# Optimization experiments

Measured on AMD Instinct MI355X. Metric: run time of the kernel, lower is better.

The kernel has to match this reference:

```python
import jax, jax.numpy as jnp
import numpy as np

B, T, N = 64, 128, 64   # batch, win_size, input_size (= node_num)
H, E, K, CS = 64, 128, 7, 8  # hidden_size, embed_size, kernel_size, control_size
NEG_SLOPE = 0.2


def _p(key, shape, scale=0.05):
    return scale * jax.random.normal(key, shape, dtype=jnp.float32)


def setup_inputs() -> dict:
    key = jax.random.key(0)
    ks = jax.random.split(key, 32)
    inp = {
        "x": jax.random.normal(ks[0], (B, T, N), dtype=jnp.float32),
        "y": jax.random.normal(ks[1], (B, T, CS), dtype=jnp.float32),
        # Conv1d(N -> N, kernel K)
        "conv_w": _p(ks[2], (N, N, K)),
        "conv_b": _p(ks[3], (N,)),
        # rnn_enc GRU: input N -> hidden H
        "We_ih": _p(ks[4], (3 * H, N)), "We_hh": _p(ks[5], (3 * H, H)),
        "be_ih": _p(ks[6], (3 * H,)), "be_hh": _p(ks[7], (3 * H,)),
        # MP_GAT linears
        "Ww": _p(ks[8], (E, 2 * T)), "bw": _p(ks[9], (E,)),
        "Wa": _p(ks[10], (1, E)), "ba": _p(ks[11], (1,)),
        # encoder GRU: input H+N -> H
        "Wm_ih": _p(ks[12], (3 * H, H + N)), "Wm_hh": _p(ks[13], (3 * H, H)),
        "bm_ih": _p(ks[14], (3 * H,)), "bm_hh": _p(ks[15], (3 * H,)),
        # rnn_dec GRU: input H -> H
        "Wd_ih": _p(ks[16], (3 * H, H)), "Wd_hh": _p(ks[17], (3 * H, H)),
        "bd_ih": _p(ks[18], (3 * H,)), "bd_hh": _p(ks[19], (3 * H,)),
        # fc_dec: H -> N
        "W_dec": _p(ks[20], (N, H)), "b_dec": _p(ks[21], (N,)),
        # fc_pred: Linear(H,N), ReLU, Linear(N,N)
        "W_p1": _p(ks[22], (N, H)), "b_p1": _p(ks[23], (N,)),
        "W_p2": _p(ks[24], (N, N)), "b_p2": _p(ks[25], (N,)),
    }
    return inp


def gru_seq(x_seq, Wih, Whh, bih, bhh):
    """torch nn.GRU (batch_first, h0=0). x_seq: [B,T,in] -> [B,T,H]."""
    gi = jnp.einsum('bti,gi->btg', x_seq, Wih) + bih  # [B,T,3H] (precompute input proj)
    h0 = jnp.zeros((x_seq.shape[0], Whh.shape[1]), x_seq.dtype)

    def step(h, gi_t):
        gh = h @ Whh.T + bhh
        i_r, i_z, i_n = jnp.split(gi_t, 3, axis=-1)
        h_r, h_z, h_n = jnp.split(gh, 3, axis=-1)
        r = jax.nn.sigmoid(i_r + h_r)
        z = jax.nn.sigmoid(i_z + h_z)
        n = jnp.tanh(i_n + r * h_n)
        h_new = (1.0 - z) * n + z * h
        return h_new, h_new

    _, hs = jax.lax.scan(step, h0, jnp.swapaxes(gi, 0, 1))
    return jnp.swapaxes(hs, 0, 1)


def _forward(x, y, conv_w, conv_b, We_ih, We_hh, be_ih, be_hh, Ww, bw, Wa, ba,
             Wm_ih, Wm_hh, bm_ih, bm_hh, Wd_ih, Wd_hh, bd_ih, bd_hh,
             W_dec, b_dec, W_p1, b_p1, W_p2, b_p2):
    # ---- CNN: pad 'same' + Conv1d + SELU. x: [B,T,N] -> channels first [B,N,T]
    pad = (K - 1) // 2
    xc = jnp.swapaxes(x, 1, 2)
    c = jax.lax.conv_general_dilated(xc, conv_w, (1,), [(pad, pad)],
                                     dimension_numbers=('NCH', 'OIH', 'NCH'))
    c = jax.nn.selu(c + conv_b[None, :, None])  # [B,N,T]
    c_btn = jnp.swapaxes(c, 1, 2)               # [B,T,N]

    # ---- rnn_enc GRU over time
    h_out = gru_seq(c_btn, We_ih, We_hh, be_ih, be_hh)  # [B,T,H]

    # ---- MP_GAT on c (v: [B, node, seq] = [B,N,T])
    v = c
    vi = jnp.broadcast_to(v[:, :, None, :], (B, N, N, T))
    vj = jnp.broadcast_to(v[:, None, :, :], (B, N, N, T))
    v_cat = jnp.concatenate([vi, vj], axis=-1)          # [B,N,N,2T]
    x_w = jax.nn.leaky_relu(jnp.einsum('bijt,et->bije', v_cat, Ww) + bw, NEG_SLOPE)
    e = (jnp.einsum('bije,oe->bijo', x_w, Wa) + ba)[..., 0]  # [B,N,N]
    attention = jax.nn.softmax(e, axis=2)
    # dropout is identity in eval mode
    h_mp = jax.nn.sigmoid(jnp.einsum('bij,bjt->bit', attention, v))  # [B,N,T]
    h_mp = jnp.swapaxes(h_mp, 1, 2)                      # [B,T,N]

    # ---- encoder / decoder GRUs (dropout = identity in eval)
    h_cat = jnp.concatenate([h_out, h_mp], axis=2)       # [B,T,H+N]
    h_enc = gru_seq(h_cat, Wm_ih, Wm_hh, bm_ih, bm_hh)
    h_dec = gru_seq(h_enc, Wd_ih, Wd_hh, bd_ih, bd_hh)

    recon = h_dec @ W_dec.T + b_dec                      # [B,T,N]
    p = jax.nn.relu(h_dec[:, 0, :] @ W_p1.T + b_p1)
    pred = p @ W_p2.T + b_p2                             # [B,N]
    return recon, pred


def reference(x, y, conv_w, conv_b, We_ih, We_hh, be_ih, be_hh, Ww, bw, Wa, ba,
              Wm_ih, Wm_hh, bm_ih, bm_hh, Wd_ih, Wd_hh, bd_ih, bd_hh,
              W_dec, b_dec, W_p1, b_p1, W_p2, b_p2):
    return _forward(x, y, conv_w, conv_b, We_ih, We_hh, be_ih, be_hh, Ww, bw, Wa, ba,
                    Wm_ih, Wm_hh, bm_ih, bm_hh, Wd_ih, Wd_hh, bd_ih, bd_hh,
                    W_dec, b_dec, W_p1, b_p1, W_p2, b_p2)
```

## Files before the change

kernel.cpp:

```cpp
#include <hip/hip_runtime.h>
#include <math.h>

#define BB 64
#define TT 128
#define NN 64
#define HH 64
#define EE 128
#define KK 7
#define GG 192

typedef _Float16 half2_t __attribute__((ext_vector_type(2)));

__device__ __forceinline__ float sigmoidf_(float x){ return 1.f/(1.f+expf(-x)); }
__device__ __forceinline__ float fsig_(float x){
  return __builtin_amdgcn_rcpf(1.f + __builtin_amdgcn_exp2f(-1.44269504f * x));
}
__device__ __forceinline__ float ftanh_(float x){
  return fmaf(-2.f, __builtin_amdgcn_rcpf(1.f + __builtin_amdgcn_exp2f(2.88539008f * x)), 1.f);
}

#define PIPE_BARRIER() asm volatile("s_waitcnt lgkmcnt(0)\ns_barrier" ::: "memory")
#define LGKM0() asm volatile("s_waitcnt lgkmcnt(0)" ::: "memory")

__device__ __forceinline__ void loadrow_(float* d, const float* src){
  const float4* p = (const float4*)src;
  #pragma unroll
  for (int i = 0; i < 16; ++i) {
    float4 v = p[i];
    d[4*i] = v.x; d[4*i+1] = v.y; d[4*i+2] = v.z; d[4*i+3] = v.w;
  }
}
__device__ __forceinline__ void loadroww_(half2_t* d, const float* src){
  const float4* p = (const float4*)src;
  #pragma unroll
  for (int i = 0; i < 16; ++i) {
    float4 v = p[i];
    d[2*i]   = half2_t{(_Float16)v.x, (_Float16)v.y};
    d[2*i+1] = half2_t{(_Float16)v.z, (_Float16)v.w};
  }
}

__global__ void conv_selu_kernel(const float* __restrict__ x, const float* __restrict__ w,
                                 const float* __restrict__ bias,
                                 float* __restrict__ c_nt, float* __restrict__ c_btn) {
  const int og = blockIdx.x, b = blockIdx.y, t = threadIdx.x;
  const int o0 = og * 8;
  __shared__ __align__(16) float xs[NN][TT + 1];
  __shared__ __align__(16) float ws[NN * KK][8];
  for (int idx = t; idx < TT * NN; idx += 128) {
    int tt = idx >> 6, nn = idx & 63;
    xs[nn][tt] = x[(size_t)(b * TT + tt) * NN + nn];
  }
  for (int idx = t; idx < NN * KK * 8; idx += 128) {
    int oo = idx & 7, ik = idx >> 3;
    ws[ik][oo] = w[(size_t)(o0 + oo) * (NN * KK) + ik];
  }
  __syncthreads();
  float acc[8];
  #pragma unroll
  for (int oo = 0; oo < 8; ++oo) acc[oo] = bias[o0 + oo];
  for (int i = 0; i < NN; ++i) {
    #pragma unroll
    for (int k = 0; k < KK; ++k) {
      int tt = t + k - 3;
      if (tt >= 0 && tt < TT) {
        float xv = xs[i][tt];
        const float* wp = &ws[i * KK + k][0];
        float4 w0 = *(const float4*)wp;
        float4 w1 = *(const float4*)(wp + 4);
        acc[0] += xv * w0.x; acc[1] += xv * w0.y; acc[2] += xv * w0.z; acc[3] += xv * w0.w;
        acc[4] += xv * w1.x; acc[5] += xv * w1.y; acc[6] += xv * w1.z; acc[7] += xv * w1.w;
      }
    }
  }
  const float alpha = 1.6732632423543772f, scale = 1.0507009873554805f;
  #pragma unroll
  for (int oo = 0; oo < 8; ++oo) {
    float a = acc[oo];
    float r = a > 0.f ? scale * a : scale * alpha * expm1f(a);
    int o = o0 + oo;
    c_nt[((size_t)b * NN + o) * TT + t] = r;
    c_btn[((size_t)b * TT + t) * NN + o] = r;
  }
}

__global__ void s12_kernel(const float* __restrict__ c_nt, const float* __restrict__ Ww,
                           float* __restrict__ s1, float* __restrict__ s2) {
  const int m0 = blockIdx.x * 16, col = threadIdx.x;
  __shared__ __align__(16) float ins[16][TT];
  for (int idx = col; idx < 16 * TT; idx += 128) {
    int r = idx >> 7, k = idx & 127;
    ins[r][k] = c_nt[(size_t)(m0 + r) * TT + k];
  }
  __syncthreads();
  const float* w1 = Ww + (size_t)col * (2 * TT);
  const float* w2 = w1 + TT;
  float acc1[16], acc2[16];
  #pragma unroll
  for (int r = 0; r < 16; ++r) { acc1[r] = 0.f; acc2[r] = 0.f; }
  #pragma unroll 2
  for (int k = 0; k < TT; k += 4) {
    float4 wv1 = *(const float4*)(w1 + k);
    float4 wv2 = *(const float4*)(w2 + k);
    #pragma unroll
    for (int r = 0; r < 16; ++r) {
      float4 iv = *(const float4*)&ins[r][k];
      acc1[r] += iv.x * wv1.x + iv.y * wv1.y + iv.z * wv1.z + iv.w * wv1.w;
      acc2[r] += iv.x * wv2.x + iv.y * wv2.y + iv.z * wv2.z + iv.w * wv2.w;
    }
  }
  #pragma unroll
  for (int r = 0; r < 16; ++r) {
    s1[(size_t)(m0 + r) * EE + col] = acc1[r];
    s2[(size_t)(m0 + r) * EE + col] = acc2[r];
  }
}

__global__ void gat_kernel(const float* __restrict__ s1, const float* __restrict__ s2,
                           const float* __restrict__ bw, const float* __restrict__ Wa,
                           const float* __restrict__ ba, const float* __restrict__ c_nt,
                           float* __restrict__ hmp) {
  const int it = blockIdx.x, b = blockIdx.y, tid = threadIdx.x;
  const int i0 = it * 16;
  __shared__ float s2s[NN][EE + 1];
  __shared__ float s1b[16][EE];
  __shared__ float cs[NN][TT + 1];
  __shared__ float was[EE];
  __shared__ float att[16][NN];
  for (int idx = tid; idx < NN * EE; idx += 256) {
    int j = idx >> 7, e = idx & 127;
    s2s[j][e] = s2[((size_t)b * NN + j) * EE + e] + bw[e];
  }
  for (int idx = tid; idx < 16 * EE; idx += 256) {
    int r = idx >> 7, e = idx & 127;
    s1b[r][e] = s1[((size_t)b * NN + i0 + r) * EE + e];
  }
  for (int idx = tid; idx < NN * TT; idx += 256) {
    int j = idx >> 7, t = idx & 127;
    cs[j][t] = c_nt[((size_t)b * NN + j) * TT + t];
  }
  if (tid < EE) was[tid] = Wa[tid];
  __syncthreads();
  const int wv = tid >> 6, j = tid & 63;
  #pragma unroll
  for (int pass = 0; pass < 4; ++pass) {
    const int il = pass * 4 + wv;
    float acc = 0.f;
    #pragma unroll 8
    for (int e = 0; e < EE; ++e) {
      float v = s1b[il][e] + s2s[j][e];
      v = v > 0.f ? v : 0.2f * v;
      acc += was[e] * v;
    }
    float ej = acc + ba[0];
    float mx = ej;
    for (int off = 32; off >= 1; off >>= 1) mx = fmaxf(mx, __shfl_xor(mx, off));
    float ex = __builtin_amdgcn_exp2f(1.44269504f * (ej - mx));
    float sm = ex;
    for (int off = 32; off >= 1; off >>= 1) sm += __shfl_xor(sm, off);
    att[il][j] = ex / sm;
  }
  __syncthreads();
  for (int o = tid; o < 16 * TT; o += 256) {
    int il = o >> 7, t = o & 127;
    float acc = 0.f;
    #pragma unroll 8
    for (int jj = 0; jj < NN; ++jj) acc += att[il][jj] * cs[jj][t];
    hmp[((size_t)b * TT + t) * NN + i0 + il] = sigmoidf_(acc);
  }
}

__global__ __launch_bounds__(256, 1)
void fused_chain4(const float* __restrict__ c_btn, const float* __restrict__ hmp,
                  const float* __restrict__ We_ih, const float* __restrict__ be_ih,
                  const float* __restrict__ We_hh, const float* __restrict__ be_hh,
                  const float* __restrict__ Wm_ih, const float* __restrict__ bm_ih,
                  const float* __restrict__ Wm_hh, const float* __restrict__ bm_hh,
                  const float* __restrict__ Wd_ih, const float* __restrict__ bd_ih,
                  const float* __restrict__ Wd_hh, const float* __restrict__ bd_hh,
                  const float* __restrict__ W_dec, const float* __restrict__ b_dec,
                  const float* __restrict__ W_p1, const float* __restrict__ b_p1,
                  const float* __restrict__ W_p2, const float* __restrict__ b_p2,
                  float* __restrict__ recon, float* __restrict__ pred) {
  const int b = blockIdx.x, tid = threadIdx.x, wid = tid >> 6, g = tid & 63;
  __shared__ __align__(16) _Float16 cbuf[HH], mbuf[HH], h3h[HH];
  __shared__ __align__(16) _Float16 h1h[2][HH], h2h[2][HH];
  __shared__ __align__(16) float q2[2][GG], h3f[2][HH];
  __shared__ __align__(16) float h0s[HH], ps[HH];

  half2_t wxa[32], wxb[32], wxc[32];
  half2_t wya[32], wyb[32], wyc[32];
  float wdec[64];
  float b0 = 0.f, b1 = 0.f, b2 = 0.f, e0 = 0.f, e1 = 0.f, e2 = 0.f, bdc = 0.f;
  if (wid == 0) {
    loadroww_(wxa, We_ih + (size_t)g * HH);
    loadroww_(wxb, We_ih + (size_t)(g + 64) * HH);
    loadroww_(wxc, We_ih + (size_t)(g + 128) * HH);
    loadroww_(wya, We_hh + (size_t)g * HH);
    loadroww_(wyb, We_hh + (size_t)(g + 64) * HH);
    loadroww_(wyc, We_hh + (size_t)(g + 128) * HH);
    b0 = be_ih[g]; b1 = be_ih[64 + g]; b2 = be_ih[128 + g];
    e0 = be_hh[g]; e1 = be_hh[64 + g]; e2 = be_hh[128 + g];
  } else if (wid == 1) {
    loadroww_(wxa, Wm_ih + (size_t)g * 128);
    loadroww_(wxb, Wm_ih + (size_t)(g + 64) * 128);
    loadroww_(wxc, Wm_ih + (size_t)(g + 128) * 128);
    loadroww_(wya, Wm_ih + (size_t)g * 128 + 64);
    loadroww_(wyb, Wm_ih + (size_t)(g + 64) * 128 + 64);
    loadroww_(wyc, Wm_ih + (size_t)(g + 128) * 128 + 64);
    b0 = bm_ih[g]; b1 = bm_ih[64 + g]; b2 = bm_ih[128 + g];
  } else if (wid == 2) {
    loadroww_(wxa, Wm_hh + (size_t)g * HH);
    loadroww_(wxb, Wm_hh + (size_t)(g + 64) * HH);
    loadroww_(wxc, Wm_hh + (size_t)(g + 128) * HH);
    loadrow_(wdec, W_dec + (size_t)g * HH);
    b0 = bm_hh[g]; b1 = bm_hh[64 + g]; b2 = bm_hh[128 + g];
    bdc = b_dec[g];
  } else {
    loadroww_(wxa, Wd_ih + (size_t)g * HH);
    loadroww_(wxb, Wd_ih + (size_t)(g + 64) * HH);
    loadroww_(wxc, Wd_ih + (size_t)(g + 128) * HH);
    loadroww_(wya, Wd_hh + (size_t)g * HH);
    loadroww_(wyb, Wd_hh + (size_t)(g + 64) * HH);
    loadroww_(wyc, Wd_hh + (size_t)(g + 128) * HH);
    b0 = bd_ih[g]; b1 = bd_ih[64 + g]; b2 = bd_ih[128 + g];
    e0 = bd_hh[g]; e1 = bd_hh[64 + g]; e2 = bd_hh[128 + g];
  }
  if (wid == 0) {
    h1h[0][g] = (_Float16)0.f; h1h[1][g] = (_Float16)0.f;
    h2h[0][g] = (_Float16)0.f; h2h[1][g] = (_Float16)0.f;
    h3h[g]    = (_Float16)0.f;
  }
  const float* cb = c_btn + (size_t)b * TT * NN + g;
  const float* hm = hmp   + (size_t)b * TT * NN + g;
  float cc = 0.f, cn = 0.f;
  if (wid == 0) { cc = cb[0]; cn = cb[NN]; }
  if (wid == 1) { cc = hm[0]; cn = hm[NN]; }
  float hown = 0.f;
  __syncthreads();

  for (int p = 0; p < TT + 4; ++p) {
    const int pw = p & 1, pr = pw ^ 1;
    if (wid == 0) {
      int t = p;
      if (t < TT) {
        cbuf[g] = (_Float16)cc;
        float cl = 0.f;
        if (t + 2 < TT) cl = cb[(size_t)(t + 2) * NN];
        LGKM0();
        float a0 = b0, a1 = b1, a2 = b2, r0 = e0, r1 = e1, r2 = e2;
        const float4* c4 = (const float4*)&cbuf[0];
        const float4* h4 = (const float4*)&h1h[pr][0];
        #pragma unroll
        for (int ch = 0; ch < 8; ++ch) {
          float4 cv = c4[ch], hv = h4[ch];
          const half2_t* cq = (const half2_t*)&cv;
          const half2_t* hq = (const half2_t*)&hv;
          #pragma unroll
          for (int k = 0; k < 4; ++k) {
            int i = 4 * ch + k;
            a0 = __builtin_amdgcn_fdot2(cq[k], wxa[i], a0, false);
            a1 = __builtin_amdgcn_fdot2(cq[k], wxb[i], a1, false);
            a2 = __builtin_amdgcn_fdot2(cq[k], wxc[i], a2, false);
            r0 = __builtin_amdgcn_fdot2(hq[k], wya[i], r0, false);
            r1 = __builtin_amdgcn_fdot2(hq[k], wyb[i], r1, false);
            r2 = __builtin_amdgcn_fdot2(hq[k], wyc[i], r2, false);
          }
        }
        float r = fsig_(a0 + r0), z = fsig_(a1 + r1), n = ftanh_(a2 + r * r2);
        hown = fmaf(z, hown - n, n);
        h1h[pw][g] = (_Float16)hown;
        cc = cn; cn = cl;
      }
    } else if (wid == 1) {
      int t = p - 1;
      if (t >= 0 && t < TT) {
        mbuf[g] = (_Float16)cc;
        float cl = 0.f;
        if (t + 2 < TT) cl = hm[(size_t)(t + 2) * NN];
        LGKM0();
        float a0 = b0, a1 = b1, a2 = b2, r0 = 0.f, r1 = 0.f, r2 = 0.f;
        const float4* h4 = (const float4*)&h1h[pr][0];
        const float4* m4 = (const float4*)&mbuf[0];
        #pragma unroll
        for (int ch = 0; ch < 8; ++ch) {
          float4 hv = h4[ch], mv = m4[ch];
          const half2_t* hq = (const half2_t*)&hv;
          const half2_t* mq = (const half2_t*)&mv;
          #pragma unroll
          for (int k = 0; k < 4; ++k) {
            int i = 4 * ch + k;
            a0 = __builtin_amdgcn_fdot2(hq[k], wxa[i], a0, false);
            a1 = __builtin_amdgcn_fdot2(hq[k], wxb[i], a1, false);
            a2 = __builtin_amdgcn_fdot2(hq[k], wxc[i], a2, false);
            r0 = __builtin_amdgcn_fdot2(mq[k], wya[i], r0, false);
            r1 = __builtin_amdgcn_fdot2(mq[k], wyb[i], r1, false);
            r2 = __builtin_amdgcn_fdot2(mq[k], wyc[i], r2, false);
          }
        }
        q2[pw][g] = a0 + r0; q2[pw][64 + g] = a1 + r1; q2[pw][128 + g] = a2 + r2;
        cc = cn; cn = cl;
      }
    } else if (wid == 2) {
      int t = p - 2;
      if (t >= 0 && t < TT) {
        float a0 = b0, a1 = b1, a2 = b2;
        const float4* h4 = (const float4*)&h2h[pr][0];
        #pragma unroll
        for (int ch = 0; ch < 8; ++ch) {
          float4 hv = h4[ch];
          const half2_t* hq = (const half2_t*)&hv;
          #pragma unroll
          for (int k = 0; k < 4; ++k) {
            int i = 4 * ch + k;
            a0 = __builtin_amdgcn_fdot2(hq[k], wxa[i], a0, false);
            a1 = __builtin_amdgcn_fdot2(hq[k], wxb[i], a1, false);
            a2 = __builtin_amdgcn_fdot2(hq[k], wxc[i], a2, false);
          }
        }
        float r = fsig_(q2[pr][g] + a0), z = fsig_(q2[pr][64 + g] + a1);
        float n = ftanh_(q2[pr][128 + g] + r * a2);
        hown = fmaf(z, hown - n, n);
        h2h[pw][g] = (_Float16)hown;
      }
      int t4 = p - 4;
      if (t4 >= 0) {
        const float4* h4 = (const float4*)&h3f[pr][0];
        float a0 = bdc, a1 = 0.f;
        #pragma unroll
        for (int i = 0; i < 8; ++i) {
          float4 hv = h4[2 * i], hw = h4[2 * i + 1];
          a0 = fmaf(hv.x, wdec[8*i],   fmaf(hv.y, wdec[8*i+1], fmaf(hv.z, wdec[8*i+2], fmaf(hv.w, wdec[8*i+3], a0))));
          a1 = fmaf(hw.x, wdec[8*i+4], fmaf(hw.y, wdec[8*i+5], fmaf(hw.z, wdec[8*i+6], fmaf(hw.w, wdec[8*i+7], a1))));
        }
        recon[((size_t)b * TT + t4) * NN + g] = a0 + a1;
      }
    } else {
      int t = p - 3;
      if (t >= 0 && t < TT) {
        float a0 = b0, a1 = b1, a2 = b2, r0 = e0, r1 = e1, r2 = e2;
        const float4* h4 = (const float4*)&h2h[pr][0];
        const float4* o4 = (const float4*)&h3h[0];
        #pragma unroll
        for (int ch = 0; ch < 8; ++ch) {
          float4 hv = h4[ch], ov = o4[ch];
          const half2_t* hq = (const half2_t*)&hv;
          const half2_t* oq = (const half2_t*)&ov;
          #pragma unroll
          for (int k = 0; k < 4; ++k) {
            int i = 4 * ch + k;
            a0 = __builtin_amdgcn_fdot2(hq[k], wxa[i], a0, false);
            a1 = __builtin_amdgcn_fdot2(hq[k], wxb[i], a1, false);
            a2 = __builtin_amdgcn_fdot2(hq[k], wxc[i], a2, false);
            r0 = __builtin_amdgcn_fdot2(oq[k], wya[i], r0, false);
            r1 = __builtin_amdgcn_fdot2(oq[k], wyb[i], r1, false);
            r2 = __builtin_amdgcn_fdot2(oq[k], wyc[i], r2, false);
          }
        }
        float r = fsig_(a0 + r0), z = fsig_(a1 + r1), n = ftanh_(a2 + r * r2);
        hown = fmaf(z, hown - n, n);
        h3h[g] = (_Float16)hown;
        h3f[pw][g] = hown;
        if (t == 0) h0s[g] = hown;
      }
    }
    PIPE_BARRIER();
  }

  if (wid == 2) {
    float w1r[64]; loadrow_(w1r, W_p1 + (size_t)g * HH);
    const float4* h4 = (const float4*)&h0s[0];
    float a = b_p1[g];
    #pragma unroll
    for (int i = 0; i < 16; ++i) {
      float4 hv = h4[i];
      a = fmaf(hv.x, w1r[4*i], fmaf(hv.y, w1r[4*i+1], fmaf(hv.z, w1r[4*i+2], fmaf(hv.w, w1r[4*i+3], a))));
    }
    ps[g] = fmaxf(a, 0.f);
    LGKM0();
    float w2r[64]; loadrow_(w2r, W_p2 + (size_t)g * HH);
    const float4* p4 = (const float4*)&ps[0];
    float c2 = b_p2[g];
    #pragma unroll
    for (int i = 0; i < 16; ++i) {
      float4 pv = p4[i];
      c2 = fmaf(pv.x, w2r[4*i], fmaf(pv.y, w2r[4*i+1], fmaf(pv.z, w2r[4*i+2], fmaf(pv.w, w2r[4*i+3], c2))));
    }
    pred[(size_t)b * NN + g] = c2;
  }
}

extern "C" void kernel_launch(void* const* d_in, const int* in_sizes, int n_in,
                              void* d_out, int out_size, void* d_ws, size_t ws_size,
                              hipStream_t stream) {
  const float* x      = (const float*)d_in[0];
  const float* conv_w = (const float*)d_in[2];
  const float* conv_b = (const float*)d_in[3];
  const float* We_ih  = (const float*)d_in[4];
  const float* We_hh  = (const float*)d_in[5];
  const float* be_ih  = (const float*)d_in[6];
  const float* be_hh  = (const float*)d_in[7];
  const float* Ww     = (const float*)d_in[8];
  const float* bw     = (const float*)d_in[9];
  const float* Wa     = (const float*)d_in[10];
  const float* ba     = (const float*)d_in[11];
  const float* Wm_ih  = (const float*)d_in[12];
  const float* Wm_hh  = (const float*)d_in[13];
  const float* bm_ih  = (const float*)d_in[14];
  const float* bm_hh  = (const float*)d_in[15];
  const float* Wd_ih  = (const float*)d_in[16];
  const float* Wd_hh  = (const float*)d_in[17];
  const float* bd_ih  = (const float*)d_in[18];
  const float* bd_hh  = (const float*)d_in[19];
  const float* W_dec  = (const float*)d_in[20];
  const float* b_dec  = (const float*)d_in[21];
  const float* W_p1   = (const float*)d_in[22];
  const float* b_p1   = (const float*)d_in[23];
  const float* W_p2   = (const float*)d_in[24];
  const float* b_p2   = (const float*)d_in[25];
  float* out = (float*)d_out;

  float* wsf   = (float*)d_ws;
  float* c_nt  = wsf;
  float* c_btn = c_nt  + 524288;
  float* s1    = c_btn + 524288;
  float* s2    = s1    + 524288;
  float* hmp   = s2    + 524288;

  conv_selu_kernel<<<dim3(8, BB), 128, 0, stream>>>(x, conv_w, conv_b, c_nt, c_btn);
  s12_kernel<<<BB * NN / 16, 128, 0, stream>>>(c_nt, Ww, s1, s2);
  gat_kernel<<<dim3(4, BB), 256, 0, stream>>>(s1, s2, bw, Wa, ba, c_nt, hmp);
  fused_chain4<<<BB, 256, 0, stream>>>(c_btn, hmp,
                                       We_ih, be_ih, We_hh, be_hh,
                                       Wm_ih, bm_ih, Wm_hh, bm_hh,
                                       Wd_ih, bd_ih, Wd_hh, bd_hh,
                                       W_dec, b_dec, W_p1, b_p1, W_p2, b_p2,
                                       out, out + BB * TT * NN);
}
```

Measured before the change: 212.0 us.

## Process four timesteps per barrier phase in the fused GRU wavefront pipeline

The four-wave pipelined GRU chain now advances in chunks of four timesteps per block-wide barrier instead of one. This cuts the number of s_barrier phases from about TT+4 to about TT/4+4. Within a chunk, the serial waves read their own previous step from LDS with only an lgkmcnt wait, not a full barrier. Shared buffers grow to hold four steps per phase. The cost is a longer pipeline fill/drain and more LDS traffic per phase.

```diff
diff --git a/kernel.cpp b/kernel.cpp
--- a/kernel.cpp
+++ b/kernel.cpp
@@ -37,6 +37,46 @@
     float4 v = p[i];
     d[2*i]   = half2_t{(_Float16)v.x, (_Float16)v.y};
     d[2*i+1] = half2_t{(_Float16)v.z, (_Float16)v.w};
+  }
+}
+__device__ __forceinline__ void mv6_(const _Float16* xs, const _Float16* ys,
+    const half2_t* wxa, const half2_t* wxb, const half2_t* wxc,
+    const half2_t* wya, const half2_t* wyb, const half2_t* wyc,
+    float& a0, float& a1, float& a2, float& r0, float& r1, float& r2){
+  const float4* x4 = (const float4*)xs;
+  const float4* y4 = (const float4*)ys;
+  #pragma unroll
+  for (int ch = 0; ch < 8; ++ch) {
+    float4 xv = x4[ch], yv = y4[ch];
+    const half2_t* xq = (const half2_t*)&xv;
+    const half2_t* yq = (const half2_t*)&yv;
+    #pragma unroll
+    for (int k = 0; k < 4; ++k) {
+      int i = 4 * ch + k;
+      a0 = __builtin_amdgcn_fdot2(xq[k], wxa[i], a0, false);
+      a1 = __builtin_amdgcn_fdot2(xq[k], wxb[i], a1, false);
+      a2 = __builtin_amdgcn_fdot2(xq[k], wxc[i], a2, false);
+      r0 = __builtin_amdgcn_fdot2(yq[k], wya[i], r0, false);
+      r1 = __builtin_amdgcn_fdot2(yq[k], wyb[i], r1, false);
+      r2 = __builtin_amdgcn_fdot2(yq[k], wyc[i], r2, false);
+    }
+  }
+}
+__device__ __forceinline__ void mv3_(const _Float16* xs,
+    const half2_t* wxa, const half2_t* wxb, const half2_t* wxc,
+    float& a0, float& a1, float& a2){
+  const float4* x4 = (const float4*)xs;
+  #pragma unroll
+  for (int ch = 0; ch < 8; ++ch) {
+    float4 xv = x4[ch];
+    const half2_t* xq = (const half2_t*)&xv;
+    #pragma unroll
+    for (int k = 0; k < 4; ++k) {
+      int i = 4 * ch + k;
+      a0 = __builtin_amdgcn_fdot2(xq[k], wxa[i], a0, false);
+      a1 = __builtin_amdgcn_fdot2(xq[k], wxb[i], a1, false);
+      a2 = __builtin_amdgcn_fdot2(xq[k], wxc[i], a2, false);
+    }
   }
 }
 
@@ -170,23 +210,40 @@
   }
 }
 
+#define K4 4
 __global__ __launch_bounds__(256, 1)
-void fused_chain4(const float* __restrict__ c_btn, const float* __restrict__ hmp,
-                  const float* __restrict__ We_ih, const float* __restrict__ be_ih,
-                  const float* __restrict__ We_hh, const float* __restrict__ be_hh,
-                  const float* __restrict__ Wm_ih, const float* __restrict__ bm_ih,
-                  const float* __restrict__ Wm_hh, const float* __restrict__ bm_hh,
-                  const float* __restrict__ Wd_ih, const float* __restrict__ bd_ih,
-                  const float* __restrict__ Wd_hh, const float* __restrict__ bd_hh,
-                  const float* __restrict__ W_dec, const float* __restrict__ b_dec,
-                  const float* __restrict__ W_p1, const float* __restrict__ b_p1,
-                  const float* __restrict__ W_p2, const float* __restrict__ b_p2,
-                  float* __restrict__ recon, float* __restrict__ pred) {
+void fused_chain4k(const float* __restrict__ c_btn, const float* __restrict__ hmp,
+                   const float* __restrict__ We_ih, const float* __restrict__ be_ih,
+                   const float* __restrict__ We_hh, const float* __restrict__ be_hh,
+                   const float* __restrict__ Wm_ih, const float* __restrict__ bm_ih,
+                   const float* __restrict__ Wm_hh, const float* __restrict__ bm_hh,
+                   const float* __restrict__ Wd_ih, const float* __restrict__ bd_ih,
+                   const float* __restrict__ Wd_hh, const float* __restrict__ bd_hh,
+                   const float* __restrict__ W_dec, const float* __restrict__ b_dec,
+                   const float* __restrict__ W_p1, const float* __restrict__ b_p1,
+                   const float* __restrict__ W_p2, const float* __restrict__ b_p2,
+                   float* __restrict__ recon, float* __restrict__ pred) {
   const int b = blockIdx.x, tid = threadIdx.x, wid = tid >> 6, g = tid & 63;
-  __shared__ __align__(16) _Float16 cbuf[HH], mbuf[HH], h3h[HH];
-  __shared__ __align__(16) _Float16 h1h[2][HH], h2h[2][HH];
-  __shared__ __align__(16) float q2[2][GG], h3f[2][HH];
+  __shared__ __align__(16) _Float16 cbuf[2][K4][HH], mbuf[2][K4][HH];
+  __shared__ __align__(16) _Float16 h1h[2][K4][HH], h2h[2][K4][HH], h3h[2][K4][HH];
+  __shared__ __align__(16) float q2[2][K4][GG], h3f[2][K4][HH];
   __shared__ __align__(16) float h0s[HH], ps[HH];
+
+  {
+    _Float16* z1 = &h1h[0][0][0];
+    _Float16* z2 = &h2h[0][0][0];
+    _Float16* z3 = &h3h[0][0][0];
+    _Float16* z4 = &cbuf[0][0][0];
+    _Float16* z5 = &mbuf[0][0][0];
+    for (int idx = tid; idx < 2 * K4 * HH; idx += 256) {
+      z1[idx] = (_Float16)0.f; z2[idx] = (_Float16)0.f; z3[idx] = (_Float16)0.f;
+      z4[idx] = (_Float16)0.f; z5[idx] = (_Float16)0.f;
+    }
+    float* zf = &h3f[0][0][0];
+    for (int idx = tid; idx < 2 * K4 * HH; idx += 256) zf[idx] = 0.f;
+    float* zq = &q2[0][0][0];
+    for (int idx = tid; idx < 2 * K4 * GG; idx += 256) zq[idx] = 0.f;
+  }
 
   half2_t wxa[32], wxb[32], wxc[32];
   half2_t wya[32], wyb[32], wyc[32];
@@ -226,142 +283,109 @@
     b0 = bd_ih[g]; b1 = bd_ih[64 + g]; b2 = bd_ih[128 + g];
     e0 = bd_hh[g]; e1 = bd_hh[64 + g]; e2 = bd_hh[128 + g];
   }
-  if (wid == 0) {
-    h1h[0][g] = (_Float16)0.f; h1h[1][g] = (_Float16)0.f;
-    h2h[0][g] = (_Float16)0.f; h2h[1][g] = (_Float16)0.f;
-    h3h[g]    = (_Float16)0.f;
-  }
   const float* cb = c_btn + (size_t)b * TT * NN + g;
   const float* hm = hmp   + (size_t)b * TT * NN + g;
-  float cc = 0.f, cn = 0.f;
-  if (wid == 0) { cc = cb[0]; cn = cb[NN]; }
-  if (wid == 1) { cc = hm[0]; cn = hm[NN]; }
+  float cur[K4], nxt[K4];
+  #pragma unroll
+  for (int s = 0; s < K4; ++s) { cur[s] = 0.f; nxt[s] = 0.f; }
+  if (wid == 0) {
+    #pragma unroll
+    for (int s = 0; s < K4; ++s) cur[s] = cb[(size_t)s * NN];
+  }
+  if (wid == 1) {
+    #pragma unroll
+    for (int s = 0; s < K4; ++s) cur[s] = hm[(size_t)s * NN];
+  }
   float hown = 0.f;
   __syncthreads();
 
-  for (int p = 0; p < TT + 4; ++p) {
+  const int NPH = TT / K4 + 4;
+  for (int p = 0; p < NPH; ++p) {
     const int pw = p & 1, pr = pw ^ 1;
     if (wid == 0) {
-      int t = p;
-      if (t < TT) {
-        cbuf[g] = (_Float16)cc;
-        float cl = 0.f;
-        if (t + 2 < TT) cl = cb[(size_t)(t + 2) * NN];
+      if (p <= TT / K4 - 1) {
+        const int t0 = p * K4;
+        #pragma unroll
+        for (int s = 0; s < K4; ++s) cbuf[pw][s][g] = (_Float16)cur[s];
+        #pragma unroll
+        for (int s = 0; s < K4; ++s)
+          nxt[s] = (t0 + K4 + s < TT) ? cb[(size_t)(t0 + K4 + s) * NN] : 0.f;
+        #pragma unroll
+        for (int s = 0; s < K4; ++s) {
+          const _Float16* hp = (s == 0) ? &h1h[pr][K4-1][0] : &h1h[pw][s-1][0];
+          LGKM0();
+          float a0 = b0, a1 = b1, a2 = b2, r0 = e0, r1 = e1, r2 = e2;
+          mv6_(&cbuf[pw][s][0], hp, wxa, wxb, wxc, wya, wyb, wyc, a0, a1, a2, r0, r1, r2);
+          float r = fsig_(a0 + r0), z = fsig_(a1 + r1), n = ftanh_(a2 + r * r2);
+          hown = fmaf(z, hown - n, n);
+          h1h[pw][s][g] = (_Float16)hown;
+        }
+        #pragma unroll
+        for (int s = 0; s < K4; ++s) cur[s] = nxt[s];
+      }
+    } else if (wid == 1) {
+      if (p >= 1 && p <= TT / K4) {
+        const int t0 = p * K4;
+        #pragma unroll
+        for (int s = 0; s < K4; ++s) mbuf[pw][s][g] = (_Float16)cur[s];
+        #pragma unroll
+        for (int s = 0; s < K4; ++s)
+          nxt[s] = (t0 + s < TT) ? hm[(size_t)(t0 + s) * NN] : 0.f;
         LGKM0();
-        float a0 = b0, a1 = b1, a2 = b2, r0 = e0, r1 = e1, r2 = e2;
-        const float4* c4 = (const float4*)&cbuf[0];
-        const float4* h4 = (const float4*)&h1h[pr][0];
-        #pragma unroll
-        for (int ch = 0; ch < 8; ++ch) {
-          float4 cv = c4[ch], hv = h4[ch];
-          const half2_t* cq = (const half2_t*)&cv;
-          const half2_t* hq = (const half2_t*)&hv;
+        #pragma unroll
+        for (int s = 0; s < K4; ++s) {
+          float a0 = b0, a1 = b1, a2 = b2, r0 = 0.f, r1 = 0.f, r2 = 0.f;
+          mv6_(&h1h[pr][s][0], &mbuf[pw][s][0], wxa, wxb, wxc, wya, wyb, wyc,
+               a0, a1, a2, r0, r1, r2);
+          q2[pw][s][g] = a0 + r0; q2[pw][s][64 + g] = a1 + r1; q2[pw][s][128 + g] = a2 + r2;
+        }
+        #pragma unroll
+        for (int s = 0; s < K4; ++s) cur[s] = nxt[s];
+      }
+    } else if (wid == 2) {
+      if (p >= 2 && p <= TT / K4 + 1) {
+        #pragma unroll
+        for (int s = 0; s < K4; ++s) {
+          const _Float16* hp = (s == 0) ? &h2h[pr][K4-1][0] : &h2h[pw][s-1][0];
+          LGKM0();
+          float a0 = b0, a1 = b1, a2 = b2;
+          mv3_(hp, wxa, wxb, wxc, a0, a1, a2);
+          float r = fsig_(q2[pr][s][g] + a0), z = fsig_(q2[pr][s][64 + g] + a1);
+          float n = ftanh_(q2[pr][s][128 + g] + r * a2);
+          hown = fmaf(z, hown - n, n);
+          h2h[pw][s][g] = (_Float16)hown;
+        }
+      }
+      if (p >= 4) {
+        #pragma unroll
+        for (int s = 0; s < K4; ++s) {
+          int t4 = (p - 4) * K4 + s;
+          const float4* h4 = (const float4*)&h3f[pr][s][0];
+          float a0 = bdc, a1 = 0.f;
           #pragma unroll
-          for (int k = 0; k < 4; ++k) {
-            int i = 4 * ch + k;
-            a0 = __builtin_amdgcn_fdot2(cq[k], wxa[i], a0, false);
-            a1 = __builtin_amdgcn_fdot2(cq[k], wxb[i], a1, false);
-            a2 = __builtin_amdgcn_fdot2(cq[k], wxc[i], a2, false);
-            r0 = __builtin_amdgcn_fdot2(hq[k], wya[i], r0, false);
-            r1 = __builtin_amdgcn_fdot2(hq[k], wyb[i], r1, false);
-            r2 = __builtin_amdgcn_fdot2(hq[k], wyc[i], r2, false);
+          for (int i = 0; i < 8; ++i) {
+            float4 hv = h4[2 * i], hw = h4[2 * i + 1];
+            a0 = fmaf(hv.x, wdec[8*i],   fmaf(hv.y, wdec[8*i+1], fmaf(hv.z, wdec[8*i+2], fmaf(hv.w, wdec[8*i+3], a0))));
+            a1 = fmaf(hw.x, wdec[8*i+4], fmaf(hw.y, wdec[8*i+5], fmaf(hw.z, wdec[8*i+6], fmaf(hw.w, wdec[8*i+7], a1))));
           }
+          recon[((size_t)b * TT + t4) * NN + g] = a0 + a1;
         }
-        float r = fsig_(a0 + r0), z = fsig_(a1 + r1), n = ftanh_(a2 + r * r2);
-        hown = fmaf(z, hown - n, n);
-        h1h[pw][g] = (_Float16)hown;
-        cc = cn; cn = cl;
-      }
-    } else if (wid == 1) {
-      int t = p - 1;
-      if (t >= 0 && t < TT) {
-        mbuf[g] = (_Float16)cc;
-        float cl = 0.f;
-        if (t + 2 < TT) cl = hm[(size_t)(t + 2) * NN];
-        LGKM0();
-        float a0 = b0, a1 = b1, a2 = b2, r0 = 0.f, r1 = 0.f, r2 = 0.f;
-        const float4* h4 = (const float4*)&h1h[pr][0];
-        const float4* m4 = (const float4*)&mbuf[0];
-        #pragma unroll
-        for (int ch = 0; ch < 8; ++ch) {
-          float4 hv = h4[ch], mv = m4[ch];
-          const half2_t* hq = (const half2_t*)&hv;
-          const half2_t* mq = (const half2_t*)&mv;
-          #pragma unroll
-          for (int k = 0; k < 4; ++k) {
-            int i = 4 * ch + k;
-            a0 = __builtin_amdgcn_fdot2(hq[k], wxa[i], a0, false);
-            a1 = __builtin_amdgcn_fdot2(hq[k], wxb[i], a1, false);
-            a2 = __builtin_amdgcn_fdot2(hq[k], wxc[i], a2, false);
-            r0 = __builtin_amdgcn_fdot2(mq[k], wya[i], r0, false);
-            r1 = __builtin_amdgcn_fdot2(mq[k], wyb[i], r1, false);
-            r2 = __builtin_amdgcn_fdot2(mq[k], wyc[i], r2, false);
-          }
+      }
+    } else {
+      if (p >= 3 && p <= TT / K4 + 2) {
+        const int t0 = (p - 3) * K4;
+        #pragma unroll
+        for (int s = 0; s < K4; ++s) {
+          const _Float16* op = (s == 0) ? &h3h[pr][K4-1][0] : &h3h[pw][s-1][0];
+          LGKM0();
+          float a0 = b0, a1 = b1, a2 = b2, r0 = e0, r1 = e1, r2 = e2;
+          mv6_(&h2h[pr][s][0], op, wxa, wxb, wxc, wya, wyb, wyc, a0, a1, a2, r0, r1, r2);
+          float r = fsig_(a0 + r0), z = fsig_(a1 + r1), n = ftanh_(a2 + r * r2);
+          hown = fmaf(z, hown - n, n);
+          h3h[pw][s][g] = (_Float16)hown;
+          h3f[pw][s][g] = hown;
+          if (t0 + s == 0) h0s[g] = hown;
         }
-        q2[pw][g] = a0 + r0; q2[pw][64 + g] = a1 + r1; q2[pw][128 + g] = a2 + r2;
-        cc = cn; cn = cl;
-      }
-    } else if (wid == 2) {
-      int t = p - 2;
-      if (t >= 0 && t < TT) {
-        float a0 = b0, a1 = b1, a2 = b2;
-        const float4* h4 = (const float4*)&h2h[pr][0];
-        #pragma unroll
-        for (int ch = 0; ch < 8; ++ch) {
-          float4 hv = h4[ch];
-          const half2_t* hq = (const half2_t*)&hv;
-          #pragma unroll
-          for (int k = 0; k < 4; ++k) {
-            int i = 4 * ch + k;
-            a0 = __builtin_amdgcn_fdot2(hq[k], wxa[i], a0, false);
-            a1 = __builtin_amdgcn_fdot2(hq[k], wxb[i], a1, false);
-            a2 = __builtin_amdgcn_fdot2(hq[k], wxc[i], a2, false);
-          }
-        }
-        float r = fsig_(q2[pr][g] + a0), z = fsig_(q2[pr][64 + g] + a1);
-        float n = ftanh_(q2[pr][128 + g] + r * a2);
-        hown = fmaf(z, hown - n, n);
-        h2h[pw][g] = (_Float16)hown;
-      }
-      int t4 = p - 4;
-      if (t4 >= 0) {
-        const float4* h4 = (const float4*)&h3f[pr][0];
-        float a0 = bdc, a1 = 0.f;
-        #pragma unroll
-        for (int i = 0; i < 8; ++i) {
-          float4 hv = h4[2 * i], hw = h4[2 * i + 1];
-          a0 = fmaf(hv.x, wdec[8*i],   fmaf(hv.y, wdec[8*i+1], fmaf(hv.z, wdec[8*i+2], fmaf(hv.w, wdec[8*i+3], a0))));
-          a1 = fmaf(hw.x, wdec[8*i+4], fmaf(hw.y, wdec[8*i+5], fmaf(hw.z, wdec[8*i+6], fmaf(hw.w, wdec[8*i+7], a1))));
-        }
-        recon[((size_t)b * TT + t4) * NN + g] = a0 + a1;
-      }
-    } else {
-      int t = p - 3;
-      if (t >= 0 && t < TT) {
-        float a0 = b0, a1 = b1, a2 = b2, r0 = e0, r1 = e1, r2 = e2;
-        const float4* h4 = (const float4*)&h2h[pr][0];
-        const float4* o4 = (const float4*)&h3h[0];
-        #pragma unroll
-        for (int ch = 0; ch < 8; ++ch) {
-          float4 hv = h4[ch], ov = o4[ch];
-          const half2_t* hq = (const half2_t*)&hv;
-          const half2_t* oq = (const half2_t*)&ov;
-          #pragma unroll
-          for (int k = 0; k < 4; ++k) {
-            int i = 4 * ch + k;
-            a0 = __builtin_amdgcn_fdot2(hq[k], wxa[i], a0, false);
-            a1 = __builtin_amdgcn_fdot2(hq[k], wxb[i], a1, false);
-            a2 = __builtin_amdgcn_fdot2(hq[k], wxc[i], a2, false);
-            r0 = __builtin_amdgcn_fdot2(oq[k], wya[i], r0, false);
-            r1 = __builtin_amdgcn_fdot2(oq[k], wyb[i], r1, false);
-            r2 = __builtin_amdgcn_fdot2(oq[k], wyc[i], r2, false);
-          }
-        }
-        float r = fsig_(a0 + r0), z = fsig_(a1 + r1), n = ftanh_(a2 + r * r2);
-        hown = fmaf(z, hown - n, n);
-        h3h[g] = (_Float16)hown;
-        h3f[pw][g] = hown;
-        if (t == 0) h0s[g] = hown;
       }
     }
     PIPE_BARRIER();
@@ -430,10 +454,10 @@
   conv_selu_kernel<<<dim3(8, BB), 128, 0, stream>>>(x, conv_w, conv_b, c_nt, c_btn);
   s12_kernel<<<BB * NN / 16, 128, 0, stream>>>(c_nt, Ww, s1, s2);
   gat_kernel<<<dim3(4, BB), 256, 0, stream>>>(s1, s2, bw, Wa, ba, c_nt, hmp);
-  fused_chain4<<<BB, 256, 0, stream>>>(c_btn, hmp,
-                                       We_ih, be_ih, We_hh, be_hh,
-                                       Wm_ih, bm_ih, Wm_hh, bm_hh,
-                                       Wd_ih, bd_ih, Wd_hh, bd_hh,
-                                       W_dec, b_dec, W_p1, b_p1, W_p2, b_p2,
-                                       out, out + BB * TT * NN);
-}
+  fused_chain4k<<<BB, 256, 0, stream>>>(c_btn, hmp,
+                                        We_ih, be_ih, We_hh, be_hh,
+                                        Wm_ih, bm_ih, Wm_hh, bm_hh,
+                                        Wd_ih, bd_ih, Wd_hh, bd_hh,
+                                        W_dec, b_dec, W_p1, b_p1, W_p2, b_p2,
+                                        out, out + BB * TT * NN);
+}
```

Result: no change. 209.7 us (-1.1%).
